# Performance work log

Measured on AMD Instinct MI355X. Metric: run time of the kernel, lower is better.

The kernel has to match this reference:

```python
import jax, jax.numpy as jnp
import numpy as np

N_NODES = 50000
N_EDGES = 800000
N_GRAPHS = 512
IN_C, HID, OUT_C = 128, 256, 16


def _mlp(h, w1, b1, w2, b2):
    # PyG-style 2-layer MLP: Linear -> ReLU -> Linear (plain last layer)
    return jax.nn.relu(h @ w1 + b1) @ w2 + b2


def setup_inputs() -> dict:
    key = jax.random.key(0)
    ks = jax.random.split(key, 16)
    x = jax.random.normal(ks[0], (N_NODES, IN_C), dtype=jnp.float32)
    edge_index = jax.random.randint(ks[1], (2, N_EDGES), 0, N_NODES, dtype=jnp.int64)
    batch = jnp.sort(jax.random.randint(ks[2], (N_NODES,), 0, N_GRAPHS, dtype=jnp.int64))

    def lin(k, fan_in, fan_out):
        s = 1.0 / np.sqrt(fan_in)
        return jax.random.uniform(k, (fan_in, fan_out), jnp.float32, -s, s)

    inp = {"x": x, "edge_index": edge_index, "batch": batch}
    dims = [(IN_C, HID), (HID, HID), (HID, HID)]
    ki = 3
    for li, (din, dh) in enumerate(dims):
        inp[f"c{li}_w1"] = lin(ks[ki], din, dh); ki += 1
        inp[f"c{li}_b1"] = jnp.zeros((dh,), jnp.float32)
        inp[f"c{li}_w2"] = lin(ks[ki], dh, dh); ki += 1
        inp[f"c{li}_b2"] = jnp.zeros((dh,), jnp.float32)
    inp["out_w1"] = lin(ks[ki], HID, HID); ki += 1
    inp["out_b1"] = jnp.zeros((HID,), jnp.float32)
    inp["out_w2"] = lin(ks[ki], HID, OUT_C); ki += 1
    inp["out_b2"] = jnp.zeros((OUT_C,), jnp.float32)
    return inp


def reference(x, edge_index, batch,
              c0_w1, c0_b1, c0_w2, c0_b2,
              c1_w1, c1_b1, c1_w2, c1_b2,
              c2_w1, c2_b1, c2_w2, c2_b2,
              out_w1, out_b1, out_w2, out_b2):
    src, dst = edge_index[0], edge_index[1]
    params = [(c0_w1, c0_b1, c0_w2, c0_b2),
              (c1_w1, c1_b1, c1_w2, c1_b2),
              (c2_w1, c2_b1, c2_w2, c2_b2)]
    h = x
    for (w1, b1, w2, b2) in params:
        # GINConv with eps=0: MLP(x + sum_{j in N(i)} x_j)
        agg = jax.ops.segment_sum(h[src], dst, num_segments=N_NODES)
        h = _mlp(h + agg, w1, b1, w2, b2)
        h = jax.nn.relu(h)
        # dropout: identity (eval mode)
    # global mean pool over graphs
    sums = jax.ops.segment_sum(h, batch, num_segments=N_GRAPHS)
    counts = jax.ops.segment_sum(jnp.ones((N_NODES,), h.dtype), batch, num_segments=N_GRAPHS)
    pooled = sums / jnp.maximum(counts, 1.0)[:, None]
    return _mlp(pooled, out_w1, out_b1, out_w2, out_b2)
```

## Files before the change

kernel.cpp:

```cpp
#include <hip/hip_runtime.h>

#define N_NODES 50000
#define N_EDGES 800000
#define N_GRAPHS 512
#define IN_C 128
#define HID 256
#define OUT_C 16

typedef __attribute__((ext_vector_type(8))) short short8;
typedef __attribute__((ext_vector_type(4))) float f32x4;

__device__ __forceinline__ float bf2f(unsigned short u) {
    return __uint_as_float(((unsigned int)u) << 16);
}
__device__ __forceinline__ unsigned short f2bf(float f) {
    unsigned int u = __float_as_uint(f);
    u += 0x7fff + ((u >> 16) & 1);
    return (unsigned short)(u >> 16);
}

#define PLANE_ELEMS ((long)N_NODES * 32)

struct PrepArgs {
    const float* x;
    const float* w[6];
    ushort* xbf;
    ushort* wt[6];
    int* deg;
    float* sums;
};

__global__ __launch_bounds__(256) void prep_kernel(PrepArgs a) {
    const int X4    = N_NODES * IN_C / 4;
    const int TW    = IN_C * HID;
    const int TH    = HID * HID;
    const int TBASE = X4;
    const int TEND  = TBASE + TW + 5 * TH;
    const int D4    = N_NODES / 4;
    const int DBASE = TEND;
    const int SBASE = DBASE + D4;
    const int S4    = N_GRAPHS * HID / 4;
    const long total = (long)SBASE + S4;

    long stride = (long)gridDim.x * blockDim.x;
    for (long i = (long)blockIdx.x * blockDim.x + threadIdx.x; i < total; i += stride) {
        if (i < X4) {
            float4 v = ((const float4*)a.x)[i];
            ushort4 o;
            o.x = f2bf(v.x); o.y = f2bf(v.y); o.z = f2bf(v.z); o.w = f2bf(v.w);
            long e = i * 4;
            int node = (int)(e >> 7);
            int col  = (int)(e & 127);
            long off = (long)(col >> 5) * PLANE_ELEMS + (long)node * 32 + (col & 31);
            *(ushort4*)(a.xbf + off) = o;
        } else if (i < TEND) {
            long r = i - TBASE;
            int wi, shift;
            long off;
            if (r < TW) { wi = 0; shift = 7; off = r; }
            else { r -= TW; wi = 1 + (int)(r / TH); shift = 8; off = r % TH; }
            int n = (int)(off >> shift);
            int k = (int)(off - ((long)n << shift));
            a.wt[wi][off] = f2bf(a.w[wi][(long)k * HID + n]);
        } else if (i < SBASE) {
            ((int4*)a.deg)[i - DBASE] = make_int4(0, 0, 0, 0);
        } else {
            ((float4*)a.sums)[i - SBASE] = make_float4(0.f, 0.f, 0.f, 0.f);
        }
    }
}

__global__ void deg_kernel(const int* __restrict__ dst, int* __restrict__ deg) {
    int e = blockIdx.x * blockDim.x + threadIdx.x;
    if (e < N_EDGES) atomicAdd(&deg[dst[e]], 1);
}

__global__ __launch_bounds__(256) void scan_block(const int* __restrict__ deg,
                                                  int* __restrict__ partial,
                                                  int* __restrict__ blockSums) {
    __shared__ int s[256];
    int t = threadIdx.x;
    int i = blockIdx.x * 256 + t;
    int v = (i < N_NODES) ? deg[i] : 0;
    s[t] = v;
    __syncthreads();
    #pragma unroll
    for (int off = 1; off < 256; off <<= 1) {
        int add = (t >= off) ? s[t - off] : 0;
        __syncthreads();
        s[t] += add;
        __syncthreads();
    }
    if (i < N_NODES) partial[i] = s[t] - v;
    if (t == 255) blockSums[blockIdx.x] = s[255];
}

__global__ __launch_bounds__(256) void add_offsets_fused(
    const int* __restrict__ partial, const int* __restrict__ blockSums,
    int* __restrict__ rowptr, int* __restrict__ cursor, int nb) {
    __shared__ int s[256];
    __shared__ int myOff;
    int t = threadIdx.x;
    int v = (t < nb) ? blockSums[t] : 0;
    s[t] = v;
    __syncthreads();
    #pragma unroll
    for (int off = 1; off < 256; off <<= 1) {
        int add = (t >= off) ? s[t - off] : 0;
        __syncthreads();
        s[t] += add;
        __syncthreads();
    }
    if (t == blockIdx.x) myOff = s[t] - v;
    __syncthreads();
    int i = blockIdx.x * 256 + t;
    if (i < N_NODES) {
        int r = partial[i] + myOff;
        rowptr[i] = r;
        cursor[i] = r;
    }
    if (i == 0) rowptr[N_NODES] = N_EDGES;
}

__global__ void bucket_edges(const int* __restrict__ src, const int* __restrict__ dst,
                             int* __restrict__ cursor, int* __restrict__ srcSorted) {
    int e = blockIdx.x * blockDim.x + threadIdx.x;
    if (e >= N_EDGES) return;
    int p = atomicAdd(&cursor[dst[e]], 1);
    srcSorted[p] = src[e];
}

template <int C>
__global__ __launch_bounds__(256) void gin_aggregate_planar(
    const ushort* __restrict__ hp,
    const int* __restrict__ rowptr,
    const int* __restrict__ srcIdx,
    ushort* __restrict__ out)
{
    constexpr int NC  = C / 32;
    constexpr int PER = 8 / NC;

    int b  = blockIdx.x;
    int x8 = b & 7;
    int chunk   = x8 / PER;
    int nodeblk = (b >> 3) * PER + (x8 & (PER - 1));

    int lane = threadIdx.x & 63;
    int wave = threadIdx.x >> 6;
    int grp  = lane >> 2;
    int l    = lane & 3;
    int node = nodeblk * 64 + wave * 16 + grp;
    if (node >= N_NODES) return;

    const ushort* plane = hp + (long)chunk * PLANE_ELEMS + l * 8;

    float acc[8];
    {
        short8 sv = *(const short8*)(plane + (long)node * 32);
        #pragma unroll
        for (int v = 0; v < 8; ++v) acc[v] = bf2f((unsigned short)sv[v]);
    }

    int beg = rowptr[node], end = rowptr[node + 1];
    int k = beg;
    for (; k + 8 <= end; k += 8) {
        int si[8];
        #pragma unroll
        for (int u = 0; u < 8; ++u) si[u] = srcIdx[k + u];
        short8 r[8];
        #pragma unroll
        for (int u = 0; u < 8; ++u) r[u] = *(const short8*)(plane + (long)si[u] * 32);
        #pragma unroll
        for (int u = 0; u < 8; ++u)
            #pragma unroll
            for (int v = 0; v < 8; ++v) acc[v] += bf2f((unsigned short)r[u][v]);
    }
    for (; k + 2 <= end; k += 2) {
        int si0 = srcIdx[k], si1 = srcIdx[k + 1];
        short8 r0 = *(const short8*)(plane + (long)si0 * 32);
        short8 r1 = *(const short8*)(plane + (long)si1 * 32);
        #pragma unroll
        for (int v = 0; v < 8; ++v) acc[v] += bf2f((unsigned short)r0[v]);
        #pragma unroll
        for (int v = 0; v < 8; ++v) acc[v] += bf2f((unsigned short)r1[v]);
    }
    if (k < end) {
        short8 r = *(const short8*)(plane + (long)srcIdx[k] * 32);
        #pragma unroll
        for (int v = 0; v < 8; ++v) acc[v] += bf2f((unsigned short)r[v]);
    }

    short8 o;
    #pragma unroll
    for (int v = 0; v < 8; ++v) o[v] = (short)f2bf(acc[v]);
    __builtin_nontemporal_store(o, (short8*)(out + (long)node * C + chunk * 32 + l * 8));
}

template <int K1, bool FUSE_POOL>
__global__ __launch_bounds__(512, 4) void gin_mlp(
    const ushort* __restrict__ A,
    const ushort* __restrict__ w1t,
    const float* __restrict__ b1,
    const ushort* __restrict__ w2t,
    const float* __restrict__ b2,
    ushort* __restrict__ out,
    const int* __restrict__ batch,
    float* __restrict__ sums,
    int M)
{
    __shared__ short Ls[17408];

    constexpr int NCH1 = K1 / 8;
    constexpr int NSLOT1 = 64 * NCH1;
    constexpr int NS1 = K1 / 32;

    int t = threadIdx.x;
    int lane = t & 63;
    int wv = t >> 6;
    int quad = lane >> 4;
    int l15 = lane & 15;
    int swz = l15 & 7;
    int row0 = blockIdx.x * 64;
    int col0 = wv * 32;

    short8 bw[16];
    #pragma unroll
    for (int s = 0; s < NS1; ++s)
        #pragma unroll
        for (int j = 0; j < 2; ++j)
            bw[s * 2 + j] = *(const short8*)(w1t + (long)(col0 + j * 16 + l15) * K1 + s * 32 + quad * 8);

    float bv[2];
    #pragma unroll
    for (int j = 0; j < 2; ++j) bv[j] = b1[col0 + j * 16 + l15];

    #pragma unroll
    for (int c = 0; c < NSLOT1; c += 512) {
        int s = c + t;
        int row = s / NCH1;
        int kcs = s & (NCH1 - 1);
        int kc = kcs ^ (row & 7);
        int grow = row0 + row;
        if (grow >= M) grow = M - 1;
        short8 v = *(const short8*)(A + (long)grow * K1 + kc * 8);
        *(short8*)&Ls[s * 8] = v;
    }
    __syncthreads();

    const f32x4 zero = {0.f, 0.f, 0.f, 0.f};
    f32x4 acc[4][2];
    #pragma unroll
    for (int i = 0; i < 4; ++i)
        #pragma unroll
        for (int j = 0; j < 2; ++j) acc[i][j] = zero;

    #pragma unroll
    for (int s = 0; s < NS1; ++s) {
        #pragma unroll
        for (int i = 0; i < 4; ++i) {
            int row = i * 16 + l15;
            int slot = row * NCH1 + ((s * 4 + quad) ^ swz);
            short8 a = *(const short8*)&Ls[slot * 8];
            acc[i][0] = __builtin_amdgcn_mfma_f32_16x16x32_bf16(a, bw[s * 2 + 0], acc[i][0], 0, 0, 0);
            acc[i][1] = __builtin_amdgcn_mfma_f32_16x16x32_bf16(a, bw[s * 2 + 1], acc[i][1], 0, 0, 0);
        }
    }

    #pragma unroll
    for (int s = 0; s < 8; ++s)
        #pragma unroll
        for (int j = 0; j < 2; ++j)
            bw[s * 2 + j] = *(const short8*)(w2t + (long)(col0 + j * 16 + l15) * 256 + s * 32 + quad * 8);

    __syncthreads();

    #pragma unroll
    for (int i = 0; i < 4; ++i)
        #pragma unroll
        for (int j = 0; j < 2; ++j) {
            int col = col0 + j * 16 + l15;
            int kc2 = col >> 3, sub = col & 7;
            #pragma unroll
            for (int r = 0; r < 4; ++r) {
                int row = i * 16 + quad * 4 + r;
                int slot = row * 32 + (kc2 ^ (row & 7));
                float o = fmaxf(acc[i][j][r] + bv[j], 0.f);
                Ls[slot * 8 + sub] = (short)f2bf(o);
            }
        }

    #pragma unroll
    for (int j = 0; j < 2; ++j) bv[j] = b2[col0 + j * 16 + l15];

    __syncthreads();

    #pragma unroll
    for (int i = 0; i < 4; ++i)
        #pragma unroll
        for (int j = 0; j < 2; ++j) acc[i][j] = zero;

    #pragma unroll
    for (int s = 0; s < 8; ++s) {
        #pragma unroll
        for (int i = 0; i < 4; ++i) {
            int row = i * 16 + l15;
            int slot = row * 32 + ((s * 4 + quad) ^ swz);
            short8 a = *(const short8*)&Ls[slot * 8];
            acc[i][0] = __builtin_amdgcn_mfma_f32_16x16x32_bf16(a, bw[s * 2 + 0], acc[i][0], 0, 0, 0);
            acc[i][1] = __builtin_amdgcn_mfma_f32_16x16x32_bf16(a, bw[s * 2 + 1], acc[i][1], 0, 0, 0);
        }
    }

    if constexpr (!FUSE_POOL) {
        __syncthreads();
        #pragma unroll
        for (int i = 0; i < 4; ++i)
            #pragma unroll
            for (int j = 0; j < 2; ++j) {
                int col = col0 + j * 16 + l15;
                #pragma unroll
                for (int r = 0; r < 4; ++r) {
                    int row = i * 16 + quad * 4 + r;
                    float o = fmaxf(acc[i][j][r] + bv[j], 0.f);
                    Ls[row * 272 + col] = (short)f2bf(o);
                }
            }
        __syncthreads();
        #pragma unroll
        for (int k = 0; k < 4; ++k) {
            int piece = t + k * 512;
            int chunk = piece >> 8;
            int wc    = piece & 255;
            int row   = wc >> 2;
            int g     = wc & 3;
            int grow  = row0 + row;
            if (grow < M) {
                short8 v = *(const short8*)&Ls[row * 272 + chunk * 32 + g * 8];
                *(short8*)(out + (long)chunk * PLANE_ELEMS + (long)grow * 32 + g * 8) = v;
            }
        }
    } else {
        float pacc[2];
        #pragma unroll
        for (int j = 0; j < 2; ++j) pacc[j] = 0.f;
        int cur = -1;
        #pragma unroll
        for (int i = 0; i < 4; ++i) {
            #pragma unroll
            for (int r = 0; r < 4; ++r) {
                int row = row0 + i * 16 + quad * 4 + r;
                if (row >= M) continue;
                int g = batch[row];
                if (g != cur) {
                    if (cur >= 0) {
                        #pragma unroll
                        for (int j = 0; j < 2; ++j)
                            atomicAdd(&sums[(long)cur * 256 + col0 + j * 16 + l15], pacc[j]);
                    }
                    cur = g;
                    #pragma unroll
                    for (int j = 0; j < 2; ++j) pacc[j] = 0.f;
                }
                #pragma unroll
                for (int j = 0; j < 2; ++j)
                    pacc[j] += fmaxf(acc[i][j][r] + bv[j], 0.f);
            }
        }
        if (cur >= 0) {
            #pragma unroll
            for (int j = 0; j < 2; ++j)
                atomicAdd(&sums[(long)cur * 256 + col0 + j * 16 + l15], pacc[j]);
        }
    }
}

__global__ __launch_bounds__(256) void final_mlp_kernel(
    const float* __restrict__ sums, const int* __restrict__ batch,
    const float* __restrict__ w1, const float* __restrict__ b1,
    const float* __restrict__ w2, const float* __restrict__ b2,
    float* __restrict__ out) {
    __shared__ float row[HID];
    __shared__ float hid[HID];
    __shared__ int cntS;
    int g = blockIdx.x;
    int t = threadIdx.x;
    if (t == 0) {
        int lo = 0, hi = N_NODES;
        while (lo < hi) { int m = (lo + hi) >> 1; if (batch[m] < g) lo = m + 1; else hi = m; }
        int lo2 = lo, hi2 = N_NODES;
        while (lo2 < hi2) { int m = (lo2 + hi2) >> 1; if (batch[m] < g + 1) lo2 = m + 1; else hi2 = m; }
        cntS = lo2 - lo;
    }
    __syncthreads();
    float cnt = fmaxf((float)cntS, 1.0f);
    row[t] = sums[(long)g * HID + t] / cnt;
    __syncthreads();
    float acc = b1[t];
    for (int k = 0; k < HID; ++k) acc += row[k] * w1[k * HID + t];
    hid[t] = fmaxf(acc, 0.f);
    __syncthreads();
    if (t < OUT_C) {
        float o = b2[t];
        for (int k = 0; k < HID; ++k) o += hid[k] * w2[k * OUT_C + t];
        out[(long)g * OUT_C + t] = o;
    }
}

extern "C" void kernel_launch(void* const* d_in, const int* in_sizes, int n_in,
                              void* d_out, int out_size, void* d_ws, size_t ws_size,
                              hipStream_t stream) {
    const float* x     = (const float*)d_in[0];
    const int*   ei    = (const int*)d_in[1];
    const int*   batch = (const int*)d_in[2];
    const int*   src   = ei;
    const int*   dst   = ei + N_EDGES;

    const float* c_w1[3] = { (const float*)d_in[3],  (const float*)d_in[7],  (const float*)d_in[11] };
    const float* c_b1[3] = { (const float*)d_in[4],  (const float*)d_in[8],  (const float*)d_in[12] };
    const float* c_w2[3] = { (const float*)d_in[5],  (const float*)d_in[9],  (const float*)d_in[13] };
    const float* c_b2[3] = { (const float*)d_in[6],  (const float*)d_in[10], (const float*)d_in[14] };
    const float* out_w1 = (const float*)d_in[15];
    const float* out_b1 = (const float*)d_in[16];
    const float* out_w2 = (const float*)d_in[17];
    const float* out_b2 = (const float*)d_in[18];

    char* p = (char*)d_ws;
    auto alloc = [&](size_t bytes) {
        char* r = p;
        p += (bytes + 15) & ~(size_t)15;
        return r;
    };
    ushort* xbf  = (ushort*)alloc((size_t)N_NODES * IN_C * 2);
    ushort* bufA = (ushort*)alloc((size_t)N_NODES * HID * 2);
    ushort* bufB = (ushort*)alloc((size_t)N_NODES * HID * 2);
    ushort* wt[6];
    wt[0] = (ushort*)alloc((size_t)IN_C * HID * 2);
    for (int i = 1; i < 6; ++i) wt[i] = (ushort*)alloc((size_t)HID * HID * 2);
    float* sums   = (float*)alloc((size_t)N_GRAPHS * HID * 4);
    int* deg       = (int*)alloc((size_t)N_NODES * 4);
    int* rowptr    = (int*)alloc((size_t)(N_NODES + 1) * 4);
    int* blockSums = (int*)alloc(256 * 4);
    int* cursor    = (int*)alloc((size_t)N_NODES * 4);
    int* srcSorted = (int*)alloc((size_t)N_EDGES * 4);

    const int nb = (N_NODES + 255) / 256;

    {
        PrepArgs a;
        a.x = x;
        a.w[0] = c_w1[0]; a.w[1] = c_w2[0];
        a.w[2] = c_w1[1]; a.w[3] = c_w2[1];
        a.w[4] = c_w1[2]; a.w[5] = c_w2[2];
        a.xbf = xbf;
        for (int i = 0; i < 6; ++i) a.wt[i] = wt[i];
        a.deg = deg;
        a.sums = sums;
        prep_kernel<<<2048, 256, 0, stream>>>(a);
    }

    deg_kernel<<<(N_EDGES + 255) / 256, 256, 0, stream>>>(dst, deg);
    scan_block<<<nb, 256, 0, stream>>>(deg, rowptr, blockSums);
    add_offsets_fused<<<nb, 256, 0, stream>>>(rowptr, blockSums, rowptr, cursor, nb);
    bucket_edges<<<(N_EDGES + 255) / 256, 256, 0, stream>>>(src, dst, cursor, srcSorted);

    const int nodeBlks = (N_NODES + 63) / 64;
    const int aggX128  = nodeBlks * (IN_C / 32);
    const int aggX256  = nodeBlks * (HID / 32);
    const int mlpGrid  = (N_NODES + 63) / 64;

    gin_aggregate_planar<IN_C><<<aggX128, 256, 0, stream>>>(xbf, rowptr, srcSorted, bufB);
    gin_mlp<IN_C, false><<<mlpGrid, 512, 0, stream>>>(bufB, wt[0], c_b1[0], wt[1], c_b2[0],
                                                      bufA, batch, sums, N_NODES);

    gin_aggregate_planar<HID><<<aggX256, 256, 0, stream>>>(bufA, rowptr, srcSorted, bufB);
    gin_mlp<HID, false><<<mlpGrid, 512, 0, stream>>>(bufB, wt[2], c_b1[1], wt[3], c_b2[1],
                                                     bufA, batch, sums, N_NODES);

    gin_aggregate_planar<HID><<<aggX256, 256, 0, stream>>>(bufA, rowptr, srcSorted, bufB);
    gin_mlp<HID, true><<<mlpGrid, 512, 0, stream>>>(bufB, wt[4], c_b1[2], wt[5], c_b2[2],
                                                    bufA, batch, sums, N_NODES);

    final_mlp_kernel<<<N_GRAPHS, 256, 0, stream>>>(sums, batch, out_w1, out_b1,
                                                   out_w2, out_b2, (float*)d_out);
}
```

Measured before the change: 444.6 us.

## Make GIN MLP kernel persistent with register-resident weights across tiles

Turns the per-tile MLP kernel into a persistent kernel with 256 blocks, each looping over a contiguous range of 64-row tiles. Both weight matrices and biases now stay in registers for the whole kernel instead of being reloaded per tile. The staged, coalesced output write through shared memory is replaced by direct scalar bf16 stores, and the edge bucketing now uses a nontemporal store. In exchange, register pressure rises and occupancy falls (launch bounds 512,2), there is no overlap of loads with compute inside a block, and the scattered 2-byte output stores may be less efficient.

```diff
diff --git a/kernel.cpp b/kernel.cpp
--- a/kernel.cpp
+++ b/kernel.cpp
@@ -127,7 +127,7 @@
     int e = blockIdx.x * blockDim.x + threadIdx.x;
     if (e >= N_EDGES) return;
     int p = atomicAdd(&cursor[dst[e]], 1);
-    srcSorted[p] = src[e];
+    __builtin_nontemporal_store(src[e], &srcSorted[p]);
 }
 
 template <int C>
@@ -197,7 +197,7 @@
 }
 
 template <int K1, bool FUSE_POOL>
-__global__ __launch_bounds__(512, 4) void gin_mlp(
+__global__ __launch_bounds__(512, 2) void gin_mlp_persist(
     const ushort* __restrict__ A,
     const ushort* __restrict__ w1t,
     const float* __restrict__ b1,
@@ -206,13 +206,15 @@
     ushort* __restrict__ out,
     const int* __restrict__ batch,
     float* __restrict__ sums,
-    int M)
+    int M, int nTiles, int nPers)
 {
-    __shared__ short Ls[17408];
-
     constexpr int NCH1 = K1 / 8;
     constexpr int NSLOT1 = 64 * NCH1;
     constexpr int NS1 = K1 / 32;
+    constexpr int PFN = NSLOT1 / 512;
+
+    __shared__ short LsA[NSLOT1 * 8];
+    __shared__ short LsH[2048 * 8];
 
     int t = threadIdx.x;
     int lane = t & 63;
@@ -220,156 +222,145 @@
     int quad = lane >> 4;
     int l15 = lane & 15;
     int swz = l15 & 7;
-    int row0 = blockIdx.x * 64;
     int col0 = wv * 32;
 
-    short8 bw[16];
+    short8 w1r[NS1 * 2];
     #pragma unroll
     for (int s = 0; s < NS1; ++s)
         #pragma unroll
         for (int j = 0; j < 2; ++j)
-            bw[s * 2 + j] = *(const short8*)(w1t + (long)(col0 + j * 16 + l15) * K1 + s * 32 + quad * 8);
-
-    float bv[2];
-    #pragma unroll
-    for (int j = 0; j < 2; ++j) bv[j] = b1[col0 + j * 16 + l15];
-
-    #pragma unroll
-    for (int c = 0; c < NSLOT1; c += 512) {
-        int s = c + t;
-        int row = s / NCH1;
-        int kcs = s & (NCH1 - 1);
-        int kc = kcs ^ (row & 7);
-        int grow = row0 + row;
-        if (grow >= M) grow = M - 1;
-        short8 v = *(const short8*)(A + (long)grow * K1 + kc * 8);
-        *(short8*)&Ls[s * 8] = v;
-    }
-    __syncthreads();
+            w1r[s * 2 + j] = *(const short8*)(w1t + (long)(col0 + j * 16 + l15) * K1 + s * 32 + quad * 8);
+    short8 w2r[16];
+    #pragma unroll
+    for (int s = 0; s < 8; ++s)
+        #pragma unroll
+        for (int j = 0; j < 2; ++j)
+            w2r[s * 2 + j] = *(const short8*)(w2t + (long)(col0 + j * 16 + l15) * 256 + s * 32 + quad * 8);
+    float bv1[2], bv2[2];
+    #pragma unroll
+    for (int j = 0; j < 2; ++j) {
+        bv1[j] = b1[col0 + j * 16 + l15];
+        bv2[j] = b2[col0 + j * 16 + l15];
+    }
+
+    int t0 = (int)(((long)blockIdx.x * nTiles) / nPers);
+    int t1 = (int)(((long)(blockIdx.x + 1) * nTiles) / nPers);
 
     const f32x4 zero = {0.f, 0.f, 0.f, 0.f};
-    f32x4 acc[4][2];
-    #pragma unroll
-    for (int i = 0; i < 4; ++i)
-        #pragma unroll
-        for (int j = 0; j < 2; ++j) acc[i][j] = zero;
-
-    #pragma unroll
-    for (int s = 0; s < NS1; ++s) {
-        #pragma unroll
-        for (int i = 0; i < 4; ++i) {
-            int row = i * 16 + l15;
-            int slot = row * NCH1 + ((s * 4 + quad) ^ swz);
-            short8 a = *(const short8*)&Ls[slot * 8];
-            acc[i][0] = __builtin_amdgcn_mfma_f32_16x16x32_bf16(a, bw[s * 2 + 0], acc[i][0], 0, 0, 0);
-            acc[i][1] = __builtin_amdgcn_mfma_f32_16x16x32_bf16(a, bw[s * 2 + 1], acc[i][1], 0, 0, 0);
+
+    for (int ti = t0; ti < t1; ++ti) {
+        int row0 = ti * 64;
+
+        #pragma unroll
+        for (int c = 0; c < PFN; ++c) {
+            int s = c * 512 + t;
+            int row = s / NCH1;
+            int kcs = s & (NCH1 - 1);
+            int kc = kcs ^ (row & 7);
+            int grow = row0 + row;
+            if (grow >= M) grow = M - 1;
+            *(short8*)&LsA[s * 8] = *(const short8*)(A + (long)grow * K1 + kc * 8);
         }
-    }
-
-    #pragma unroll
-    for (int s = 0; s < 8; ++s)
-        #pragma unroll
-        for (int j = 0; j < 2; ++j)
-            bw[s * 2 + j] = *(const short8*)(w2t + (long)(col0 + j * 16 + l15) * 256 + s * 32 + quad * 8);
-
-    __syncthreads();
-
-    #pragma unroll
-    for (int i = 0; i < 4; ++i)
-        #pragma unroll
-        for (int j = 0; j < 2; ++j) {
-            int col = col0 + j * 16 + l15;
-            int kc2 = col >> 3, sub = col & 7;
-            #pragma unroll
-            for (int r = 0; r < 4; ++r) {
-                int row = i * 16 + quad * 4 + r;
-                int slot = row * 32 + (kc2 ^ (row & 7));
-                float o = fmaxf(acc[i][j][r] + bv[j], 0.f);
-                Ls[slot * 8 + sub] = (short)f2bf(o);
+        __syncthreads();
+
+        f32x4 acc[4][2];
+        #pragma unroll
+        for (int i = 0; i < 4; ++i)
+            #pragma unroll
+            for (int j = 0; j < 2; ++j) acc[i][j] = zero;
+
+        #pragma unroll
+        for (int s = 0; s < NS1; ++s) {
+            #pragma unroll
+            for (int i = 0; i < 4; ++i) {
+                int row = i * 16 + l15;
+                int slot = row * NCH1 + ((s * 4 + quad) ^ swz);
+                short8 a = *(const short8*)&LsA[slot * 8];
+                acc[i][0] = __builtin_amdgcn_mfma_f32_16x16x32_bf16(a, w1r[s * 2 + 0], acc[i][0], 0, 0, 0);
+                acc[i][1] = __builtin_amdgcn_mfma_f32_16x16x32_bf16(a, w1r[s * 2 + 1], acc[i][1], 0, 0, 0);
             }
         }
-
-    #pragma unroll
-    for (int j = 0; j < 2; ++j) bv[j] = b2[col0 + j * 16 + l15];
-
-    __syncthreads();
-
-    #pragma unroll
-    for (int i = 0; i < 4; ++i)
-        #pragma unroll
-        for (int j = 0; j < 2; ++j) acc[i][j] = zero;
-
-    #pragma unroll
-    for (int s = 0; s < 8; ++s) {
-        #pragma unroll
-        for (int i = 0; i < 4; ++i) {
-            int row = i * 16 + l15;
-            int slot = row * 32 + ((s * 4 + quad) ^ swz);
-            short8 a = *(const short8*)&Ls[slot * 8];
-            acc[i][0] = __builtin_amdgcn_mfma_f32_16x16x32_bf16(a, bw[s * 2 + 0], acc[i][0], 0, 0, 0);
-            acc[i][1] = __builtin_amdgcn_mfma_f32_16x16x32_bf16(a, bw[s * 2 + 1], acc[i][1], 0, 0, 0);
-        }
-    }
-
-    if constexpr (!FUSE_POOL) {
-        __syncthreads();
+        __syncthreads();
+
         #pragma unroll
         for (int i = 0; i < 4; ++i)
             #pragma unroll
             for (int j = 0; j < 2; ++j) {
                 int col = col0 + j * 16 + l15;
+                int kc2 = col >> 3, sub = col & 7;
                 #pragma unroll
                 for (int r = 0; r < 4; ++r) {
                     int row = i * 16 + quad * 4 + r;
-                    float o = fmaxf(acc[i][j][r] + bv[j], 0.f);
-                    Ls[row * 272 + col] = (short)f2bf(o);
+                    int slot = row * 32 + (kc2 ^ (row & 7));
+                    float o = fmaxf(acc[i][j][r] + bv1[j], 0.f);
+                    LsH[slot * 8 + sub] = (short)f2bf(o);
                 }
             }
         __syncthreads();
-        #pragma unroll
-        for (int k = 0; k < 4; ++k) {
-            int piece = t + k * 512;
-            int chunk = piece >> 8;
-            int wc    = piece & 255;
-            int row   = wc >> 2;
-            int g     = wc & 3;
-            int grow  = row0 + row;
-            if (grow < M) {
-                short8 v = *(const short8*)&Ls[row * 272 + chunk * 32 + g * 8];
-                *(short8*)(out + (long)chunk * PLANE_ELEMS + (long)grow * 32 + g * 8) = v;
+
+        #pragma unroll
+        for (int i = 0; i < 4; ++i)
+            #pragma unroll
+            for (int j = 0; j < 2; ++j) acc[i][j] = zero;
+
+        #pragma unroll
+        for (int s = 0; s < 8; ++s) {
+            #pragma unroll
+            for (int i = 0; i < 4; ++i) {
+                int row = i * 16 + l15;
+                int slot = row * 32 + ((s * 4 + quad) ^ swz);
+                short8 a = *(const short8*)&LsH[slot * 8];
+                acc[i][0] = __builtin_amdgcn_mfma_f32_16x16x32_bf16(a, w2r[s * 2 + 0], acc[i][0], 0, 0, 0);
+                acc[i][1] = __builtin_amdgcn_mfma_f32_16x16x32_bf16(a, w2r[s * 2 + 1], acc[i][1], 0, 0, 0);
             }
         }
-    } else {
-        float pacc[2];
-        #pragma unroll
-        for (int j = 0; j < 2; ++j) pacc[j] = 0.f;
-        int cur = -1;
-        #pragma unroll
-        for (int i = 0; i < 4; ++i) {
-            #pragma unroll
-            for (int r = 0; r < 4; ++r) {
-                int row = row0 + i * 16 + quad * 4 + r;
-                if (row >= M) continue;
-                int g = batch[row];
-                if (g != cur) {
-                    if (cur >= 0) {
+
+        if constexpr (!FUSE_POOL) {
+            #pragma unroll
+            for (int i = 0; i < 4; ++i)
+                #pragma unroll
+                for (int r = 0; r < 4; ++r) {
+                    int grow = row0 + i * 16 + quad * 4 + r;
+                    if (grow >= M) continue;
+                    #pragma unroll
+                    for (int j = 0; j < 2; ++j) {
+                        int col = col0 + j * 16 + l15;
+                        float o = fmaxf(acc[i][j][r] + bv2[j], 0.f);
+                        out[(long)(col >> 5) * PLANE_ELEMS + (long)grow * 32 + (col & 31)] = f2bf(o);
+                    }
+                }
+        } else {
+            float pacc[2];
+            #pragma unroll
+            for (int j = 0; j < 2; ++j) pacc[j] = 0.f;
+            int cur = -1;
+            #pragma unroll
+            for (int i = 0; i < 4; ++i) {
+                #pragma unroll
+                for (int r = 0; r < 4; ++r) {
+                    int row = row0 + i * 16 + quad * 4 + r;
+                    if (row >= M) continue;
+                    int g = batch[row];
+                    if (g != cur) {
+                        if (cur >= 0) {
+                            #pragma unroll
+                            for (int j = 0; j < 2; ++j)
+                                atomicAdd(&sums[(long)cur * 256 + col0 + j * 16 + l15], pacc[j]);
+                        }
+                        cur = g;
                         #pragma unroll
-                        for (int j = 0; j < 2; ++j)
-                            atomicAdd(&sums[(long)cur * 256 + col0 + j * 16 + l15], pacc[j]);
+                        for (int j = 0; j < 2; ++j) pacc[j] = 0.f;
                     }
-                    cur = g;
                     #pragma unroll
-                    for (int j = 0; j < 2; ++j) pacc[j] = 0.f;
+                    for (int j = 0; j < 2; ++j)
+                        pacc[j] += fmaxf(acc[i][j][r] + bv2[j], 0.f);
                 }
+            }
+            if (cur >= 0) {
                 #pragma unroll
                 for (int j = 0; j < 2; ++j)
-                    pacc[j] += fmaxf(acc[i][j][r] + bv[j], 0.f);
+                    atomicAdd(&sums[(long)cur * 256 + col0 + j * 16 + l15], pacc[j]);
             }
-        }
-        if (cur >= 0) {
-            #pragma unroll
-            for (int j = 0; j < 2; ++j)
-                atomicAdd(&sums[(long)cur * 256 + col0 + j * 16 + l15], pacc[j]);
         }
     }
 }
@@ -466,19 +457,19 @@
     const int nodeBlks = (N_NODES + 63) / 64;
     const int aggX128  = nodeBlks * (IN_C / 32);
     const int aggX256  = nodeBlks * (HID / 32);
-    const int mlpGrid  = (N_NODES + 63) / 64;
+    const int NPERS    = 256;
 
     gin_aggregate_planar<IN_C><<<aggX128, 256, 0, stream>>>(xbf, rowptr, srcSorted, bufB);
-    gin_mlp<IN_C, false><<<mlpGrid, 512, 0, stream>>>(bufB, wt[0], c_b1[0], wt[1], c_b2[0],
-                                                      bufA, batch, sums, N_NODES);
+    gin_mlp_persist<IN_C, false><<<NPERS, 512, 0, stream>>>(bufB, wt[0], c_b1[0], wt[1], c_b2[0],
+                                                            bufA, batch, sums, N_NODES, nodeBlks, NPERS);
 
     gin_aggregate_planar<HID><<<aggX256, 256, 0, stream>>>(bufA, rowptr, srcSorted, bufB);
-    gin_mlp<HID, false><<<mlpGrid, 512, 0, stream>>>(bufB, wt[2], c_b1[1], wt[3], c_b2[1],
-                                                     bufA, batch, sums, N_NODES);
+    gin_mlp_persist<HID, false><<<NPERS, 512, 0, stream>>>(bufB, wt[2], c_b1[1], wt[3], c_b2[1],
+                                                           bufA, batch, sums, N_NODES, nodeBlks, NPERS);
 
     gin_aggregate_planar<HID><<<aggX256, 256, 0, stream>>>(bufA, rowptr, srcSorted, bufB);
-    gin_mlp<HID, true><<<mlpGrid, 512, 0, stream>>>(bufB, wt[4], c_b1[2], wt[5], c_b2[2],
-                                                    bufA, batch, sums, N_NODES);
+    gin_mlp_persist<HID, true><<<NPERS, 512, 0, stream>>>(bufB, wt[4], c_b1[2], wt[5], c_b2[2],
+                                                          bufA, batch, sums, N_NODES, nodeBlks, NPERS);
 
     final_mlp_kernel<<<N_GRAPHS, 256, 0, stream>>>(sums, batch, out_w1, out_b1,
                                                    out_w2, out_b2, (float*)d_out);
```

After: 432.7 us. 1.03x faster.
